# Optimization experiments

Measured on AMD Instinct MI355X. Metric: run time of the kernel, lower is better.

The kernel has to match this reference:

```python
import jax, jax.numpy as jnp
import numpy as np

N = 100_000      # num nodes
E = 600_000      # num edges (before self-loops)
IN, H, C, OUT = 128, 4, 64, 1   # in_channels, heads, hidden_channels, out_channels
NEG_SLOPE = 0.2  # PyG GATConv leaky_relu slope


def setup_inputs() -> dict:
    key = jax.random.key(0)
    ks = jax.random.split(key, 12)
    init = lambda k, sh: (jax.random.normal(k, sh, jnp.float32) * 0.05)
    return {
        "x": jax.random.normal(ks[0], (N, IN), jnp.float32),
        "edge_index": jax.random.randint(ks[1], (2, E), 0, N, dtype=jnp.int32),
        # conv1: GATConv(IN -> C, heads=H, concat) -> out dim H*C
        "W1": init(ks[2], (IN, H, C)),
        "att_src1": init(ks[3], (H, C)),
        "att_dst1": init(ks[4], (H, C)),
        "b1": jnp.zeros((H * C,), jnp.float32),
        # conv2: GATConv(H*C -> C, heads=H, head-mean to match Linear(C, OUT))
        "W2": init(ks[5], (H * C, H, C)),
        "att_src2": init(ks[6], (H, C)),
        "att_dst2": init(ks[7], (H, C)),
        "b2": jnp.zeros((C,), jnp.float32),
        # PReLU (single shared parameter, torch default init 0.25)
        "prelu_a": jnp.float32(0.25),
        # level_predictor: Linear(C, OUT)
        "Wl": init(ks[8], (C, OUT)),
        "bl": jnp.zeros((OUT,), jnp.float32),
    }


def _add_self_loops(edge_index):
    loops = jnp.arange(N, dtype=edge_index.dtype)
    return jnp.concatenate([edge_index, jnp.stack([loops, loops])], axis=1)


def _gat_conv(x, src, dst, W, att_src, att_dst, bias, concat):
    # x: [N, F]; W: [F, H, C]
    h = jnp.einsum("nf,fhc->nhc", x, W)                      # [N, H, C]
    a_src = jnp.sum(h * att_src, axis=-1)                     # [N, H]
    a_dst = jnp.sum(h * att_dst, axis=-1)                     # [N, H]
    e = jax.nn.leaky_relu(a_src[src] + a_dst[dst], NEG_SLOPE)  # [Etot, H]
    # segment-softmax over incoming edges of each destination node
    m = jax.ops.segment_max(e, dst, num_segments=N)            # [N, H]
    e = jnp.exp(e - m[dst])
    denom = jax.ops.segment_sum(e, dst, num_segments=N)        # [N, H]
    alpha = e / (denom[dst] + 1e-16)                           # [Etot, H]
    out = jax.ops.segment_sum(h[src] * alpha[..., None], dst, num_segments=N)  # [N, H, C]
    out = out.reshape(N, H * C) if concat else out.mean(axis=1)
    return out + bias


def _prelu(x, a):
    return jnp.where(x >= 0, x, a * x)


def reference(x, edge_index, W1, att_src1, att_dst1, b1,
              W2, att_src2, att_dst2, b2, prelu_a, Wl, bl):
    # k-hop 'extraction' over the full node set is an identity -> full edge set.
    ei = _add_self_loops(edge_index)
    src, dst = ei[0], ei[1]
    h = _gat_conv(x, src, dst, W1, att_src1, att_dst1, b1, concat=True)   # [N, H*C]
    h = _prelu(h, prelu_a)
    h = _gat_conv(h, src, dst, W2, att_src2, att_dst2, b2, concat=False)  # [N, C]
    h = _prelu(h, prelu_a)
    return (h @ Wl + bl).squeeze(-1)                                       # [N]
```

## Files before the change

kernel.cpp:

```cpp
#include <hip/hip_runtime.h>
#include <cstdint>
#include <cstddef>

static constexpr int N_NODES = 100000;
static constexpr int N_EDGES = 600000;
static constexpr int E_TOT   = N_EDGES + N_NODES;
static constexpr float NEG_SLOPE = 0.2f;

typedef __attribute__((ext_vector_type(8))) _Float16 f16x8;
typedef __attribute__((ext_vector_type(4))) float f32x4;
typedef __attribute__((ext_vector_type(4))) _Float16 half4;

__device__ __forceinline__ float leaky(float x) { return x >= 0.f ? x : NEG_SLOPE * x; }

__device__ __forceinline__ void gload16(const void* g, void* l) {
  __builtin_amdgcn_global_load_lds(
      (const __attribute__((address_space(1))) unsigned int*)g,
      (__attribute__((address_space(3))) unsigned int*)l,
      16, 0, 0);
}


__global__ __launch_bounds__(256) void k_init_counts(int* __restrict__ counts) {
  int i = blockIdx.x * 256 + threadIdx.x;
  if (i < N_NODES) counts[i] = 1;
}

__global__ __launch_bounds__(256) void k_hist(const int* __restrict__ ei, int* __restrict__ counts) {
  int e = blockIdx.x * 256 + threadIdx.x;
  if (e < N_EDGES) atomicAdd(&counts[ei[N_EDGES + e]], 1);
}

__global__ __launch_bounds__(256) void k_scan1(const int* __restrict__ counts,
                                               int* __restrict__ partial,
                                               int* __restrict__ blockSums) {
  __shared__ int tmp[256];
  int tid = threadIdx.x;
  int i = blockIdx.x * 256 + tid;
  int v = (i < N_NODES) ? counts[i] : 0;
  tmp[tid] = v;
  __syncthreads();
  for (int off = 1; off < 256; off <<= 1) {
    int t = (tid >= off) ? tmp[tid - off] : 0;
    __syncthreads();
    tmp[tid] += t;
    __syncthreads();
  }
  if (i < N_NODES) partial[i] = tmp[tid] - v;
  if (tid == 255) blockSums[blockIdx.x] = tmp[tid];
}

__global__ __launch_bounds__(512) void k_scan2(int* __restrict__ blockSums, int nb) {
  __shared__ int tmp[512];
  int tid = threadIdx.x;
  int v = (tid < nb) ? blockSums[tid] : 0;
  tmp[tid] = v;
  __syncthreads();
  for (int off = 1; off < 512; off <<= 1) {
    int t = (tid >= off) ? tmp[tid - off] : 0;
    __syncthreads();
    tmp[tid] += t;
    __syncthreads();
  }
  if (tid < nb) blockSums[tid] = tmp[tid] - v;
}

__global__ __launch_bounds__(256) void k_scan3(const int* __restrict__ partial,
                                               const int* __restrict__ blockSums,
                                               int* __restrict__ rowptr,
                                               int* __restrict__ fill) {
  int i = blockIdx.x * 256 + threadIdx.x;
  if (i < N_NODES) {
    int v = partial[i] + blockSums[blockIdx.x];
    rowptr[i] = v;
    fill[i] = v;
  }
  if (i == 0) rowptr[N_NODES] = E_TOT;
}

__global__ __launch_bounds__(256) void k_scatter(const int* __restrict__ ei,
                                                 int* __restrict__ fill,
                                                 int* __restrict__ esrc) {
  int i = blockIdx.x * 256 + threadIdx.x;
  if (i >= E_TOT) return;
  int s, d;
  if (i < N_EDGES) { s = ei[i]; d = ei[N_EDGES + i]; }
  else             { s = i - N_EDGES; d = s; }
  int pos = atomicAdd(&fill[d], 1);
  esrc[pos] = s;
}


template <int K>
__global__ __launch_bounds__(256) void k_wconv(const float* __restrict__ W,
                                               _Float16* __restrict__ Wt) {
  int t = blockIdx.x * 256 + threadIdx.x;
  if (t >= K * 256) return;
  int k = t >> 8, c = t & 255;
  Wt[(size_t)c * K + k] = (_Float16)W[t];
}

template <int K>
__global__ __launch_bounds__(256) void k_wa(const float* __restrict__ W,
                                            const float* __restrict__ att_s,
                                            const float* __restrict__ att_d,
                                            _Float16* __restrict__ Wat) {
  int k = blockIdx.x;
  int h = threadIdx.x >> 6, c = threadIdx.x & 63;
  float wv = W[(size_t)k * 256 + h * 64 + c];
  float ps = wv * att_s[h * 64 + c];
  float pd = wv * att_d[h * 64 + c];
#pragma unroll
  for (int off = 32; off > 0; off >>= 1) {
    ps += __shfl_xor(ps, off);
    pd += __shfl_xor(pd, off);
  }
  if (c == 0) {
    Wat[(size_t)h * K + k] = (_Float16)ps;
    Wat[(size_t)(4 + h) * K + k] = (_Float16)pd;
  }
  if (threadIdx.x >= 8 && threadIdx.x < 16)
    Wat[(size_t)threadIdx.x * K + k] = (_Float16)0.f;
}


__global__ __launch_bounds__(256) void k_conv_x(const float* __restrict__ X,
                                                _Float16* __restrict__ X16) {
  size_t t = (size_t)blockIdx.x * 256 + threadIdx.x;
  float4 v = *(const float4*)&X[t * 4];
  half4 o;
  o[0] = (_Float16)v.x; o[1] = (_Float16)v.y;
  o[2] = (_Float16)v.z; o[3] = (_Float16)v.w;
  *(half4*)&X16[t * 4] = o;
}


template <int K>
__global__ __launch_bounds__(256, 3) void k_gemm_mfma(
    const _Float16* __restrict__ A, const _Float16* __restrict__ B,
    const _Float16* __restrict__ Wa,
    _Float16* __restrict__ H, float* __restrict__ asrc, float* __restrict__ adst) {
  __shared__ __align__(16) _Float16 lds[2][10240];

  const int tid = threadIdx.x;
  const int w = tid >> 6, lane = tid & 63;
  const int lhi = lane >> 4, llo = lane & 15;
  const int wrow = blockIdx.x * 64;
  const int wcol = w * 64;

  const int sr = tid >> 2;
  const int sc = (tid & 3) ^ (sr & 3);
  int ar = wrow + sr; if (ar > N_NODES - 1) ar = N_NODES - 1;
  const _Float16* gA  = &A[(size_t)ar * K + sc * 8];
  const _Float16* gB0 = &B[(size_t)(0 * 64 + sr) * K + sc * 8];
  const _Float16* gB1 = &B[(size_t)(1 * 64 + sr) * K + sc * 8];
  const _Float16* gB2 = &B[(size_t)(2 * 64 + sr) * K + sc * 8];
  const _Float16* gB3 = &B[(size_t)(3 * 64 + sr) * K + sc * 8];
  const int wb = w * 512;

  const _Float16* gW = &Wa[(size_t)llo * K + lhi * 8];

  f32x4 acc[4][4] = {};
  f32x4 acca[4] = {};

  const int ach = (lhi ^ (llo & 3)) * 8;

  auto STAGE = [&](int buf, int kc) {
    _Float16* L = lds[buf];
    gload16(gA + kc,  L + 0    + wb);
    gload16(gB0 + kc, L + 2048 + wb);
    gload16(gB1 + kc, L + 4096 + wb);
    gload16(gB2 + kc, L + 6144 + wb);
    gload16(gB3 + kc, L + 8192 + wb);
  };

  STAGE(0, 0);
  __syncthreads();

  constexpr int NT = K / 32;
  int cur = 0;
#pragma unroll 2
  for (int t = 0; t < NT; ++t) {
    if (t + 1 < NT) STAGE(cur ^ 1, (t + 1) * 32);

    f16x8 wfrag{};
    if (w == 0) wfrag = *(const f16x8*)&gW[t * 32];

    const _Float16* L = lds[cur];
    f16x8 af[4], bf[4];
#pragma unroll
    for (int rt = 0; rt < 4; ++rt)
      af[rt] = *(const f16x8*)&L[(rt * 16 + llo) * 32 + ach];
#pragma unroll
    for (int ct = 0; ct < 4; ++ct)
      bf[ct] = *(const f16x8*)&L[2048 + (wcol + ct * 16 + llo) * 32 + ach];

#pragma unroll
    for (int ct = 0; ct < 4; ++ct)
#pragma unroll
      for (int rt = 0; rt < 4; ++rt)
        acc[rt][ct] = __builtin_amdgcn_mfma_f32_16x16x32_f16(af[rt], bf[ct], acc[rt][ct], 0, 0, 0);
    if (w == 0) {
#pragma unroll
      for (int rt = 0; rt < 4; ++rt)
        acca[rt] = __builtin_amdgcn_mfma_f32_16x16x32_f16(af[rt], wfrag, acca[rt], 0, 0, 0);
    }
    __syncthreads();
    cur ^= 1;
  }

#pragma unroll
  for (int rt = 0; rt < 4; ++rt) {
    const int r0 = wrow + rt * 16 + lhi * 4;
#pragma unroll
    for (int ct = 0; ct < 4; ++ct) {
      const int cc = wcol + ct * 16 + llo;
#pragma unroll
      for (int e = 0; e < 4; ++e) {
        int r = r0 + e;
        if (r < N_NODES) H[(size_t)r * 256 + cc] = (_Float16)acc[rt][ct][e];
      }
    }
    if (w == 0 && llo < 8) {
#pragma unroll
      for (int e = 0; e < 4; ++e) {
        int r = r0 + e;
        if (r < N_NODES) {
          float v = acca[rt][e];
          if (llo < 4) asrc[(size_t)r * 4 + llo] = v;
          else         adst[(size_t)r * 4 + (llo - 4)] = v;
        }
      }
    }
  }
}


__global__ __launch_bounds__(256) void k_stats(const float4* __restrict__ asrc4,
                                               const float4* __restrict__ adst4,
                                               const int* __restrict__ rowptr,
                                               const int* __restrict__ esrc,
                                               float4* __restrict__ pbuf4,
                                               float4* __restrict__ dinv4) {
  int d = blockIdx.x * 256 + threadIdx.x;
  if (d >= N_NODES) return;
  const int beg = rowptr[d], end = rowptr[d + 1];
  const float4 ad = adst4[d];

  float4 den = make_float4(0.f, 0.f, 0.f, 0.f);
  for (int j = beg; j < end; ++j) {
    const float4 a = asrc4[esrc[j]];
    float4 p;
    p.x = __expf(leaky(a.x + ad.x));
    p.y = __expf(leaky(a.y + ad.y));
    p.z = __expf(leaky(a.z + ad.z));
    p.w = __expf(leaky(a.w + ad.w));
    den.x += p.x; den.y += p.y; den.z += p.z; den.w += p.w;
    pbuf4[j] = p;
  }
  float4 di;
  di.x = 1.f / (den.x + 1e-16f);
  di.y = 1.f / (den.y + 1e-16f);
  di.z = 1.f / (den.z + 1e-16f);
  di.w = 1.f / (den.w + 1e-16f);
  dinv4[d] = di;
}


__device__ __forceinline__ float4 gather_rows(const _Float16* __restrict__ htab,
                                              const float* __restrict__ pbuf,
                                              const int* __restrict__ esrc,
                                              int beg, int end, int lane, int myh) {
  float4 acc = make_float4(0.f, 0.f, 0.f, 0.f);
  for (int w = beg; w < end; w += 8) {
    const int cnt = end - w;
    const float pl = pbuf[(size_t)w * 4 + (lane & 31)];
    const int   sl = esrc[w + (lane & 7)];
    int   s[8];
    float p[8];
#pragma unroll
    for (int i = 0; i < 8; ++i) {
      s[i] = __shfl(sl, i);
      p[i] = __shfl(pl, i * 4 + myh);
    }
#pragma unroll
    for (int i = 1; i < 8; ++i) {
      if (i >= cnt) { s[i] = s[0]; p[i] = 0.f; }
    }
    half4 v[8];
#pragma unroll
    for (int i = 0; i < 8; ++i)
      v[i] = *(const half4*)&htab[(size_t)s[i] * 256 + 4 * lane];
#pragma unroll
    for (int i = 0; i < 8; ++i) {
      acc.x = fmaf(p[i], (float)v[i][0], acc.x);
      acc.y = fmaf(p[i], (float)v[i][1], acc.y);
      acc.z = fmaf(p[i], (float)v[i][2], acc.z);
      acc.w = fmaf(p[i], (float)v[i][3], acc.w);
    }
  }
  return acc;
}


__global__ __launch_bounds__(256) void k_agg1(const _Float16* __restrict__ h1,
                                              const float* __restrict__ pbuf,
                                              const float* __restrict__ dinv,
                                              const int* __restrict__ rowptr,
                                              const int* __restrict__ esrc,
                                              const float* __restrict__ b1,
                                              const float* __restrict__ prelu_a,
                                              _Float16* __restrict__ outp) {
  int gid = blockIdx.x * 256 + threadIdx.x;
  int dst = gid >> 6;
  int lane = threadIdx.x & 63;
  if (dst >= N_NODES) return;
  const int beg = rowptr[dst], end = rowptr[dst + 1];
  const int myh = lane >> 4;

  float4 acc = gather_rows(h1, pbuf, esrc, beg, end, lane, myh);
  const float sc = dinv[(size_t)dst * 4 + myh];
  acc.x *= sc; acc.y *= sc; acc.z *= sc; acc.w *= sc;

  const float a = prelu_a[0];
  const int c = 4 * lane;
  const float4 bv = *(const float4*)&b1[c];
  float4 r;
  r.x = acc.x + bv.x; r.x = r.x >= 0.f ? r.x : a * r.x;
  r.y = acc.y + bv.y; r.y = r.y >= 0.f ? r.y : a * r.y;
  r.z = acc.z + bv.z; r.z = r.z >= 0.f ? r.z : a * r.z;
  r.w = acc.w + bv.w; r.w = r.w >= 0.f ? r.w : a * r.w;

  half4 o;
  o[0] = (_Float16)r.x; o[1] = (_Float16)r.y;
  o[2] = (_Float16)r.z; o[3] = (_Float16)r.w;
  *(half4*)&outp[(size_t)dst * 256 + c] = o;
}


__global__ __launch_bounds__(256) void k_agg2(const _Float16* __restrict__ h2,
                                              const float* __restrict__ pbuf,
                                              const float* __restrict__ dinv,
                                              const int* __restrict__ rowptr,
                                              const int* __restrict__ esrc,
                                              const float* __restrict__ b2,
                                              const float* __restrict__ prelu_a,
                                              const float* __restrict__ Wl,
                                              const float* __restrict__ bl,
                                              float* __restrict__ out) {
  int gid = blockIdx.x * 256 + threadIdx.x;
  int dst = gid >> 6;
  int lane = threadIdx.x & 63;
  if (dst >= N_NODES) return;
  const int beg = rowptr[dst], end = rowptr[dst + 1];
  const int myh = lane >> 4;

  float4 acc = gather_rows(h2, pbuf, esrc, beg, end, lane, myh);
  const float sc = dinv[(size_t)dst * 4 + myh];
  acc.x *= sc; acc.y *= sc; acc.z *= sc; acc.w *= sc;

#pragma unroll
  for (int off = 16; off < 64; off <<= 1) {
    acc.x += __shfl_xor(acc.x, off);
    acc.y += __shfl_xor(acc.y, off);
    acc.z += __shfl_xor(acc.z, off);
    acc.w += __shfl_xor(acc.w, off);
  }

  const float a = prelu_a[0];
  const int c0 = 4 * (lane & 15);
  float4 v;
  v.x = 0.25f * acc.x + b2[c0 + 0]; v.x = v.x >= 0.f ? v.x : a * v.x;
  v.y = 0.25f * acc.y + b2[c0 + 1]; v.y = v.y >= 0.f ? v.y : a * v.y;
  v.z = 0.25f * acc.z + b2[c0 + 2]; v.z = v.z >= 0.f ? v.z : a * v.z;
  v.w = 0.25f * acc.w + b2[c0 + 3]; v.w = v.w >= 0.f ? v.w : a * v.w;

  float p = v.x * Wl[c0 + 0] + v.y * Wl[c0 + 1] + v.z * Wl[c0 + 2] + v.w * Wl[c0 + 3];
#pragma unroll
  for (int off = 1; off < 16; off <<= 1) p += __shfl_xor(p, off);

  if (lane == 0) out[dst] = p + bl[0];
}


static inline int cdiv(int a, int b) { return (a + b - 1) / b; }

extern "C" void kernel_launch(void* const* d_in, const int* in_sizes, int n_in,
                              void* d_out, int out_size, void* d_ws, size_t ws_size,
                              hipStream_t stream) {
  const float* x   = (const float*)d_in[0];
  const int*   ei  = (const int*)d_in[1];
  const float* W1  = (const float*)d_in[2];
  const float* as1 = (const float*)d_in[3];
  const float* ad1 = (const float*)d_in[4];
  const float* b1  = (const float*)d_in[5];
  const float* W2  = (const float*)d_in[6];
  const float* as2 = (const float*)d_in[7];
  const float* ad2 = (const float*)d_in[8];
  const float* b2  = (const float*)d_in[9];
  const float* pa  = (const float*)d_in[10];
  const float* Wl  = (const float*)d_in[11];
  const float* bl  = (const float*)d_in[12];
  float* out = (float*)d_out;

  char* ws = (char*)d_ws;
  size_t off = 0;
  auto alloc = [&](size_t bytes) -> void* {
    void* p = ws + off;
    off += (bytes + 255) & ~(size_t)255;
    return p;
  };

  _Float16* hbufA = (_Float16*)alloc((size_t)N_NODES * 256 * sizeof(_Float16));
  _Float16* R1 = (_Float16*)alloc((size_t)N_NODES * 256 * sizeof(_Float16));
  _Float16* x16  = R1;
  _Float16* h1p  = R1;

  float* asrc1 = (float*)alloc((size_t)N_NODES * 4 * sizeof(float));
  float* adst1 = (float*)alloc((size_t)N_NODES * 4 * sizeof(float));
  float* asrc2 = (float*)alloc((size_t)N_NODES * 4 * sizeof(float));
  float* adst2 = (float*)alloc((size_t)N_NODES * 4 * sizeof(float));
  float* pbuf  = (float*)alloc(((size_t)E_TOT * 4 + 64) * sizeof(float));
  float* dinv  = (float*)alloc((size_t)N_NODES * 4 * sizeof(float));

  _Float16* Wt1  = (_Float16*)alloc(256 * 128 * sizeof(_Float16));
  _Float16* Wat1 = (_Float16*)alloc(16 * 128 * sizeof(_Float16));
  _Float16* Wt2  = (_Float16*)alloc(256 * 256 * sizeof(_Float16));
  _Float16* Wat2 = (_Float16*)alloc(16 * 256 * sizeof(_Float16));

  int* counts  = (int*)alloc((size_t)N_NODES * sizeof(int));
  int* partial = (int*)alloc((size_t)N_NODES * sizeof(int));
  int* rowptr  = (int*)alloc((size_t)(N_NODES + 1) * sizeof(int));
  int* fill    = (int*)alloc((size_t)N_NODES * sizeof(int));
  int* esrc    = (int*)alloc(((size_t)E_TOT + 64) * sizeof(int));
  int* blockSums = (int*)alloc(2048 * sizeof(int));

  const int NB = cdiv(N_NODES, 256);

  k_init_counts<<<NB, 256, 0, stream>>>(counts);
  k_hist<<<cdiv(N_EDGES, 256), 256, 0, stream>>>(ei, counts);
  k_scan1<<<NB, 256, 0, stream>>>(counts, partial, blockSums);
  k_scan2<<<1, 512, 0, stream>>>(blockSums, NB);
  k_scan3<<<NB, 256, 0, stream>>>(partial, blockSums, rowptr, fill);
  k_scatter<<<cdiv(E_TOT, 256), 256, 0, stream>>>(ei, fill, esrc);

  k_wconv<128><<<cdiv(128 * 256, 256), 256, 0, stream>>>(W1, Wt1);
  k_wa<128><<<128, 256, 0, stream>>>(W1, as1, ad1, Wat1);
  k_wconv<256><<<cdiv(256 * 256, 256), 256, 0, stream>>>(W2, Wt2);
  k_wa<256><<<256, 256, 0, stream>>>(W2, as2, ad2, Wat2);

  k_conv_x<<<N_NODES * 128 / 4 / 256, 256, 0, stream>>>(x, x16);

  const int GEMM_GRID = cdiv(N_NODES, 64);

  k_gemm_mfma<128><<<GEMM_GRID, 256, 0, stream>>>(x16, Wt1, Wat1, hbufA, asrc1, adst1);
  k_stats<<<NB, 256, 0, stream>>>((const float4*)asrc1, (const float4*)adst1,
                                  rowptr, esrc, (float4*)pbuf, (float4*)dinv);
  k_agg1<<<N_NODES * 64 / 256, 256, 0, stream>>>(hbufA, pbuf, dinv, rowptr, esrc,
                                                 b1, pa, h1p);

  k_gemm_mfma<256><<<GEMM_GRID, 256, 0, stream>>>(h1p, Wt2, Wat2, hbufA, asrc2, adst2);
  k_stats<<<NB, 256, 0, stream>>>((const float4*)asrc2, (const float4*)adst2,
                                  rowptr, esrc, (float4*)pbuf, (float4*)dinv);
  k_agg2<<<N_NODES * 64 / 256, 256, 0, stream>>>(hbufA, pbuf, dinv, rowptr, esrc,
                                                 b2, pa, Wl, bl, out);
}
```

Measured before the change: 296.2 us.

## Merge prep kernels, place self-loops in scan, raise GEMM occupancy

Removes the count-init kernel in favour of a memset, with the self-loop +1 folded into the scan. scan3 now writes each node's self-loop entry directly, so the scatter handles only real edges. The x, W1 and W2 conversion kernels are merged into one launch, and both attention-projection launches into another. The GEMM launch bound's minimum-blocks hint goes from 3 to 4, which may cap registers. The goal is fewer kernel launches and fewer atomics, at the cost of possible register spills in the GEMM.

```diff
diff --git a/kernel.cpp b/kernel.cpp
--- a/kernel.cpp
+++ b/kernel.cpp
@@ -20,11 +20,6 @@
       16, 0, 0);
 }
 
-
-__global__ __launch_bounds__(256) void k_init_counts(int* __restrict__ counts) {
-  int i = blockIdx.x * 256 + threadIdx.x;
-  if (i < N_NODES) counts[i] = 1;
-}
 
 __global__ __launch_bounds__(256) void k_hist(const int* __restrict__ ei, int* __restrict__ counts) {
   int e = blockIdx.x * 256 + threadIdx.x;
@@ -37,7 +32,7 @@
   __shared__ int tmp[256];
   int tid = threadIdx.x;
   int i = blockIdx.x * 256 + tid;
-  int v = (i < N_NODES) ? counts[i] : 0;
+  int v = (i < N_NODES) ? counts[i] + 1 : 0;
   tmp[tid] = v;
   __syncthreads();
   for (int off = 1; off < 256; off <<= 1) {
@@ -68,12 +63,14 @@
 __global__ __launch_bounds__(256) void k_scan3(const int* __restrict__ partial,
                                                const int* __restrict__ blockSums,
                                                int* __restrict__ rowptr,
-                                               int* __restrict__ fill) {
+                                               int* __restrict__ fill,
+                                               int* __restrict__ esrc) {
   int i = blockIdx.x * 256 + threadIdx.x;
   if (i < N_NODES) {
     int v = partial[i] + blockSums[blockIdx.x];
     rowptr[i] = v;
-    fill[i] = v;
+    fill[i] = v + 1;
+    esrc[v] = i;
   }
   if (i == 0) rowptr[N_NODES] = E_TOT;
 }
@@ -82,34 +79,56 @@
                                                  int* __restrict__ fill,
                                                  int* __restrict__ esrc) {
   int i = blockIdx.x * 256 + threadIdx.x;
-  if (i >= E_TOT) return;
-  int s, d;
-  if (i < N_EDGES) { s = ei[i]; d = ei[N_EDGES + i]; }
-  else             { s = i - N_EDGES; d = s; }
+  if (i >= N_EDGES) return;
+  int s = ei[i], d = ei[N_EDGES + i];
   int pos = atomicAdd(&fill[d], 1);
   esrc[pos] = s;
 }
 
 
-template <int K>
-__global__ __launch_bounds__(256) void k_wconv(const float* __restrict__ W,
-                                               _Float16* __restrict__ Wt) {
-  int t = blockIdx.x * 256 + threadIdx.x;
-  if (t >= K * 256) return;
-  int k = t >> 8, c = t & 255;
-  Wt[(size_t)c * K + k] = (_Float16)W[t];
-}
-
-template <int K>
-__global__ __launch_bounds__(256) void k_wa(const float* __restrict__ W,
-                                            const float* __restrict__ att_s,
-                                            const float* __restrict__ att_d,
-                                            _Float16* __restrict__ Wat) {
-  int k = blockIdx.x;
+static constexpr int XB = N_NODES * 128 / 4 / 256;
+
+__global__ __launch_bounds__(256) void k_prep(const float* __restrict__ X,
+                                              _Float16* __restrict__ X16,
+                                              const float* __restrict__ W1,
+                                              _Float16* __restrict__ Wt1,
+                                              const float* __restrict__ W2,
+                                              _Float16* __restrict__ Wt2) {
+  int b = blockIdx.x;
+  if (b < XB) {
+    size_t t = (size_t)b * 256 + threadIdx.x;
+    float4 v = *(const float4*)&X[t * 4];
+    half4 o;
+    o[0] = (_Float16)v.x; o[1] = (_Float16)v.y;
+    o[2] = (_Float16)v.z; o[3] = (_Float16)v.w;
+    *(half4*)&X16[t * 4] = o;
+  } else if (b < XB + 128) {
+    int t = (b - XB) * 256 + threadIdx.x;
+    int k = t >> 8, c = t & 255;
+    Wt1[(size_t)c * 128 + k] = (_Float16)W1[t];
+  } else {
+    int t = (b - XB - 128) * 256 + threadIdx.x;
+    int k = t >> 8, c = t & 255;
+    Wt2[(size_t)c * 256 + k] = (_Float16)W2[t];
+  }
+}
+
+__global__ __launch_bounds__(256) void k_wa(const float* __restrict__ W1,
+                                            const float* __restrict__ as1,
+                                            const float* __restrict__ ad1,
+                                            _Float16* __restrict__ Wat1,
+                                            const float* __restrict__ W2,
+                                            const float* __restrict__ as2,
+                                            const float* __restrict__ ad2,
+                                            _Float16* __restrict__ Wat2) {
+  int b = blockIdx.x;
+  const float *W, *as, *adp; _Float16* Wat; int K, k;
+  if (b < 128) { W = W1; as = as1; adp = ad1; Wat = Wat1; K = 128; k = b; }
+  else         { W = W2; as = as2; adp = ad2; Wat = Wat2; K = 256; k = b - 128; }
   int h = threadIdx.x >> 6, c = threadIdx.x & 63;
   float wv = W[(size_t)k * 256 + h * 64 + c];
-  float ps = wv * att_s[h * 64 + c];
-  float pd = wv * att_d[h * 64 + c];
+  float ps = wv * as[h * 64 + c];
+  float pd = wv * adp[h * 64 + c];
 #pragma unroll
   for (int off = 32; off > 0; off >>= 1) {
     ps += __shfl_xor(ps, off);
@@ -124,19 +143,8 @@
 }
 
 
-__global__ __launch_bounds__(256) void k_conv_x(const float* __restrict__ X,
-                                                _Float16* __restrict__ X16) {
-  size_t t = (size_t)blockIdx.x * 256 + threadIdx.x;
-  float4 v = *(const float4*)&X[t * 4];
-  half4 o;
-  o[0] = (_Float16)v.x; o[1] = (_Float16)v.y;
-  o[2] = (_Float16)v.z; o[3] = (_Float16)v.w;
-  *(half4*)&X16[t * 4] = o;
-}
-
-
 template <int K>
-__global__ __launch_bounds__(256, 3) void k_gemm_mfma(
+__global__ __launch_bounds__(256, 4) void k_gemm_mfma(
     const _Float16* __restrict__ A, const _Float16* __restrict__ B,
     const _Float16* __restrict__ Wa,
     _Float16* __restrict__ H, float* __restrict__ asrc, float* __restrict__ adst) {
@@ -437,19 +445,15 @@
 
   const int NB = cdiv(N_NODES, 256);
 
-  k_init_counts<<<NB, 256, 0, stream>>>(counts);
+  hipMemsetAsync(counts, 0, (size_t)N_NODES * sizeof(int), stream);
   k_hist<<<cdiv(N_EDGES, 256), 256, 0, stream>>>(ei, counts);
   k_scan1<<<NB, 256, 0, stream>>>(counts, partial, blockSums);
   k_scan2<<<1, 512, 0, stream>>>(blockSums, NB);
-  k_scan3<<<NB, 256, 0, stream>>>(partial, blockSums, rowptr, fill);
-  k_scatter<<<cdiv(E_TOT, 256), 256, 0, stream>>>(ei, fill, esrc);
-
-  k_wconv<128><<<cdiv(128 * 256, 256), 256, 0, stream>>>(W1, Wt1);
-  k_wa<128><<<128, 256, 0, stream>>>(W1, as1, ad1, Wat1);
-  k_wconv<256><<<cdiv(256 * 256, 256), 256, 0, stream>>>(W2, Wt2);
-  k_wa<256><<<256, 256, 0, stream>>>(W2, as2, ad2, Wat2);
-
-  k_conv_x<<<N_NODES * 128 / 4 / 256, 256, 0, stream>>>(x, x16);
+  k_scan3<<<NB, 256, 0, stream>>>(partial, blockSums, rowptr, fill, esrc);
+  k_scatter<<<cdiv(N_EDGES, 256), 256, 0, stream>>>(ei, fill, esrc);
+
+  k_prep<<<XB + 128 + 256, 256, 0, stream>>>(x, x16, W1, Wt1, W2, Wt2);
+  k_wa<<<128 + 256, 256, 0, stream>>>(W1, as1, ad1, Wat1, W2, as2, ad2, Wat2);
 
   const int GEMM_GRID = cdiv(N_NODES, 64);
 
```

After: 296.8 us. Within noise of the previous version (+0.2%).
